# Kernel optimization log

Hardware: AMD Instinct MI355X
Metric: run time of the kernel (lower is better)

## Reference

```python
import jax, jax.numpy as jnp
import numpy as np

H = 16          # num_heads
D = 4           # att_size (hard-coded in module)
HID = 256       # hidden_size
B, N = 4, 1024
SCALE = D ** (-0.5)
BN_EPS = 1e-5
NEG_SLOPE = 0.2


def setup_inputs() -> dict:
    key = jax.random.key(0)
    ks = jax.random.split(key, 12)
    s = 0.05
    return {
        "q": jax.random.normal(ks[0], (B, HID, N), jnp.float32),
        "k": jax.random.normal(ks[1], (B, HID, N), jnp.float32),
        "v": jax.random.normal(ks[2], (B, HID, N), jnp.float32),
        "attn_bias": jax.random.normal(ks[3], (B, H, N, N), jnp.float32),
        # 1x1 Conv1d weights (kernel dim squeezed): [out_ch, in_ch]
        "Wq": jax.random.normal(ks[4], (H * D, HID), jnp.float32) * s,
        "Wk": jax.random.normal(ks[5], (H * D, HID), jnp.float32) * s,
        "Wv": jax.random.normal(ks[6], (H * D, HID), jnp.float32) * s,
        "Wo": jax.random.normal(ks[7], (HID, H * D), jnp.float32) * s,
        "bo": jax.random.normal(ks[8], (HID,), jnp.float32) * s,
        "gamma": jnp.ones((HID,), jnp.float32),
        "beta": jnp.zeros((HID,), jnp.float32),
        "run_mean": jnp.zeros((HID,), jnp.float32),
        "run_var": jnp.ones((HID,), jnp.float32),
    }


def reference(q, k, v, attn_bias, Wq, Wk, Wv, Wo, bo, gamma, beta, run_mean, run_var):
    # 1x1 conv projections: [B, HID, N] -> [B, H*D, N]
    qp = jnp.einsum('oc,bcn->bon', Wq, q)
    kp = jnp.einsum('oc,bcn->bon', Wk, k)
    vp = jnp.einsum('oc,bcn->bon', Wv, v)
    # faithful (non-standard) view: [B, H*D, N] -> [B, D, N, H]
    qh = qp.reshape(B, D, N, H).transpose(0, 3, 2, 1)   # [B, H, N, D]
    vh = vp.reshape(B, D, N, H).transpose(0, 3, 2, 1)   # [B, H, N, D]
    kh = kp.reshape(B, D, N, H).transpose(0, 3, 1, 2)   # [B, H, D, N]
    # scaled dot-product attention with additive bias
    scores = jnp.einsum('bhnd,bhdm->bhnm', qh, kh) * SCALE + attn_bias
    attn = jax.nn.softmax(scores, axis=-1)              # dropout rate 0.0 (eval)
    x = jnp.einsum('bhnm,bhmd->bhnd', attn, vh)         # [B, H, N, D]
    # transpose(3,2) then view(B, H*D, N)
    x = x.transpose(0, 1, 3, 2).reshape(B, H * D, N)
    # output 1x1 conv + BatchNorm1d (eval, running stats) + LeakyReLU(0.2)
    y = jnp.einsum('oc,bcn->bon', Wo, x) + bo[None, :, None]
    inv = jax.lax.rsqrt(run_var + BN_EPS)
    y = (y - run_mean[None, :, None]) * (gamma * inv)[None, :, None] + beta[None, :, None]
    return jnp.where(y > 0, y, NEG_SLOPE * y)
```

## Files before the change

### kernel.cpp

```cpp
#include <hip/hip_runtime.h>

#define HID 256
#define NSEQ 1024
#define NH 16
#define DH 4
#define NB 4
#define SCALEF 0.5f
#define HEADSZ (NB * NH * NSEQ * DH)

typedef float f4 __attribute__((ext_vector_type(4)));

__global__ __launch_bounds__(256) void proj_kernel(
    const float* __restrict__ q, const float* __restrict__ k,
    const float* __restrict__ v, const float* __restrict__ Wq,
    const float* __restrict__ Wk, const float* __restrict__ Wv,
    float* __restrict__ ws)
{
    const int tid   = threadIdx.x;
    const int pos_l = tid & 63;
    int cb = tid >> 6;
    cb = __builtin_amdgcn_readfirstlane(cb);
    const int p    = blockIdx.y;
    const int b    = blockIdx.z;
    const int pos0 = blockIdx.x * 64;

    const float* in = (p == 0) ? q : (p == 1) ? k : v;
    const float* W  = (p == 0) ? Wq : (p == 1) ? Wk : Wv;
    float* dst = ws + (size_t)p * HEADSZ;

    __shared__ float lds_in[64][64];

    float acc[16];
#pragma unroll
    for (int j = 0; j < 16; ++j) acc[j] = 0.f;

    const float* inb = in + (size_t)b * HID * NSEQ;

    for (int chunk = 0; chunk < 4; ++chunk) {
        const int i0 = chunk * 64;
#pragma unroll
        for (int t = 0; t < 16; ++t) {
            int e = tid + t * 256;
            int r = e >> 6, pp = e & 63;
            lds_in[r][pp] = inb[(i0 + r) * NSEQ + pos0 + pp];
        }
        __syncthreads();
#pragma unroll
        for (int i8 = 0; i8 < 64; i8 += 8) {
            float x[8];
#pragma unroll
            for (int j = 0; j < 8; ++j) x[j] = lds_in[i8 + j][pos_l];
#pragma unroll
            for (int kk = 0; kk < 16; ++kk) {
                const float* wr = W + (cb * 16 + kk) * HID + i0 + i8;
#pragma unroll
                for (int j = 0; j < 8; ++j)
                    acc[kk] = fmaf(wr[j], x[j], acc[kk]);
            }
        }
        __syncthreads();
    }

    const int pos_g = pos0 + pos_l;
    const int h     = pos_g & 15;
    const int nsub  = pos_g >> 4;
#pragma unroll
    for (int kk = 0; kk < 16; ++kk) {
        int c = cb * 16 + kk;
        int d = c >> 4;
        int n = (c & 15) * 64 + nsub;
        dst[(((size_t)b * NH + h) * NSEQ + n) * DH + d] = acc[kk];
    }
}

__global__ __launch_bounds__(256, 4) void attn_kernel(
    const float* __restrict__ bias, const float* __restrict__ ws,
    float* __restrict__ x2)
{
    const int tid  = threadIdx.x;
    const int lane = tid & 63;
    const int wave = tid >> 6;
    const int qg   = lane >> 4;
    const int kg   = lane & 15;
    const int h    = blockIdx.y;
    const int b    = blockIdx.z;
    const int n0   = blockIdx.x * 64 + wave * 16;

    const float4* Qh = (const float4*)(ws);
    const float4* Kh = (const float4*)(ws + (size_t)1 * HEADSZ);
    const float4* Vh = (const float4*)(ws + (size_t)2 * HEADSZ);
    const int headbase = (b * NH + h) * NSEQ;

    float4 q4[4];
#pragma unroll
    for (int r = 0; r < 4; ++r) q4[r] = Qh[headbase + n0 + qg * 4 + r];

    float sum[4];
    float o[4][4];
#pragma unroll
    for (int r = 0; r < 4; ++r) {
        sum[r] = 0.f;
#pragma unroll
        for (int d = 0; d < 4; ++d) o[r][d] = 0.f;
    }

    const float* bbase =
        bias + ((size_t)headbase + n0 + qg * 4) * NSEQ + kg * 4;
    const int kvbase = headbase + kg * 4;

#define LOG2E 1.44269504f
#define EOFF  (-16.f * LOG2E)

    for (int m0 = 0; m0 < NSEQ; m0 += 64) {
        f4 bb[4];
#pragma unroll
        for (int r = 0; r < 4; ++r)
            bb[r] = __builtin_nontemporal_load(
                (const f4*)(bbase + (size_t)r * NSEQ + m0));
        float4 kb[4], vb[4];
#pragma unroll
        for (int i = 0; i < 4; ++i) {
            kb[i] = Kh[kvbase + m0 + i];
            vb[i] = Vh[kvbase + m0 + i];
        }
#pragma unroll
        for (int r = 0; r < 4; ++r) {
            const float be[4] = {bb[r].x, bb[r].y, bb[r].z, bb[r].w};
#pragma unroll
            for (int i = 0; i < 4; ++i) {
                float dot = q4[r].x * kb[i].x + q4[r].y * kb[i].y +
                            q4[r].z * kb[i].z + q4[r].w * kb[i].w;
                float s = fmaf(dot, SCALEF, be[i]);
                float e = exp2f(fmaf(s, LOG2E, EOFF));
                sum[r] += e;
                o[r][0] = fmaf(e, vb[i].x, o[r][0]);
                o[r][1] = fmaf(e, vb[i].y, o[r][1]);
                o[r][2] = fmaf(e, vb[i].z, o[r][2]);
                o[r][3] = fmaf(e, vb[i].w, o[r][3]);
            }
        }
    }

#pragma unroll
    for (int st = 1; st <= 8; st <<= 1) {
#pragma unroll
        for (int r = 0; r < 4; ++r) {
            sum[r]  += __shfl_xor(sum[r],  st, 64);
            o[r][0] += __shfl_xor(o[r][0], st, 64);
            o[r][1] += __shfl_xor(o[r][1], st, 64);
            o[r][2] += __shfl_xor(o[r][2], st, 64);
            o[r][3] += __shfl_xor(o[r][3], st, 64);
        }
    }

    if (kg < 4) {
        float4 wv;
        wv.x = o[0][kg] / sum[0];
        wv.y = o[1][kg] / sum[1];
        wv.z = o[2][kg] / sum[2];
        wv.w = o[3][kg] / sum[3];
        *(float4*)(x2 + ((size_t)b * (NH * DH) + h * DH + kg) * NSEQ
                      + n0 + qg * 4) = wv;
    }
}

__global__ __launch_bounds__(256) void out_kernel(
    const float* __restrict__ x2, const float* __restrict__ Wo,
    const float* __restrict__ bo, const float* __restrict__ gamma,
    const float* __restrict__ beta, const float* __restrict__ rmean,
    const float* __restrict__ rvar, float* __restrict__ out)
{
    const int pos = blockIdx.x * 256 + threadIdx.x;
    const int o0  = blockIdx.y * 8;
    const int b   = blockIdx.z;

    float acc[8];
#pragma unroll
    for (int j = 0; j < 8; ++j) acc[j] = 0.f;

    const float* xb = x2 + (size_t)b * (NH * DH) * NSEQ;
#pragma unroll 8
    for (int c = 0; c < NH * DH; ++c) {
        float x = xb[c * NSEQ + pos];
#pragma unroll
        for (int j = 0; j < 8; ++j)
            acc[j] = fmaf(Wo[(o0 + j) * (NH * DH) + c], x, acc[j]);
    }
#pragma unroll
    for (int j = 0; j < 8; ++j) {
        int o = o0 + j;
        float inv = rsqrtf(rvar[o] + 1e-5f);
        float y = acc[j] + bo[o];
        y = (y - rmean[o]) * (gamma[o] * inv) + beta[o];
        y = (y > 0.f) ? y : 0.2f * y;
        out[((size_t)b * HID + o) * NSEQ + pos] = y;
    }
}

extern "C" void kernel_launch(void* const* d_in, const int* in_sizes, int n_in,
                              void* d_out, int out_size, void* d_ws, size_t ws_size,
                              hipStream_t stream) {
    const float* q     = (const float*)d_in[0];
    const float* k     = (const float*)d_in[1];
    const float* v     = (const float*)d_in[2];
    const float* bias  = (const float*)d_in[3];
    const float* Wq    = (const float*)d_in[4];
    const float* Wk    = (const float*)d_in[5];
    const float* Wv    = (const float*)d_in[6];
    const float* Wo    = (const float*)d_in[7];
    const float* bo    = (const float*)d_in[8];
    const float* gamma = (const float*)d_in[9];
    const float* beta  = (const float*)d_in[10];
    const float* rmean = (const float*)d_in[11];
    const float* rvar  = (const float*)d_in[12];

    float* ws = (float*)d_ws;
    float* x2 = ws + (size_t)3 * HEADSZ;
    float* out = (float*)d_out;

    proj_kernel<<<dim3(NSEQ / 64, 3, NB), 256, 0, stream>>>(q, k, v, Wq, Wk, Wv, ws);
    attn_kernel<<<dim3(NSEQ / 64, NH, NB), 256, 0, stream>>>(bias, ws, x2);
    out_kernel<<<dim3(NSEQ / 256, HID / 8, NB), 256, 0, stream>>>(
        x2, Wo, bo, gamma, beta, rmean, rvar, out);
}
```

Baseline: 123.3 us.

## Prefetch bias and projection inputs, vectorize loads in proj and output kernels

The projection kernel now loads its input tile with float4 reads and prefetches the next 64-row chunk into registers while it computes on the current one. The attention kernel double-buffers the attn_bias loads one iteration ahead and lowers the launch-bounds occupancy hint from 4 to 3 to make room for the extra registers. The output kernel is rewritten so each thread handles 4 positions with vector loads and stores across 4 output channels per block. The goal is to hide memory latency on the bandwidth-bound bias stream and to issue fewer, wider memory accesses, at the cost of higher register pressure and lower occupancy in the attention kernel.

New measurement: 135.1 us. 9.6% more time.

```diff
diff --git a/kernel.cpp b/kernel.cpp
--- a/kernel.cpp
+++ b/kernel.cpp
@@ -18,8 +18,7 @@
 {
     const int tid   = threadIdx.x;
     const int pos_l = tid & 63;
-    int cb = tid >> 6;
-    cb = __builtin_amdgcn_readfirstlane(cb);
+    int cb = __builtin_amdgcn_readfirstlane(tid >> 6);
     const int p    = blockIdx.y;
     const int b    = blockIdx.z;
     const int pos0 = blockIdx.x * 64;
@@ -30,21 +29,30 @@
 
     __shared__ float lds_in[64][64];
 
+    const int row_l = tid >> 4;
+    const int col4  = tid & 15;
+    const float* inb = in + (size_t)b * HID * NSEQ + pos0;
+
     float acc[16];
 #pragma unroll
     for (int j = 0; j < 16; ++j) acc[j] = 0.f;
 
-    const float* inb = in + (size_t)b * HID * NSEQ;
-
-    for (int chunk = 0; chunk < 4; ++chunk) {
-        const int i0 = chunk * 64;
-#pragma unroll
-        for (int t = 0; t < 16; ++t) {
-            int e = tid + t * 256;
-            int r = e >> 6, pp = e & 63;
-            lds_in[r][pp] = inb[(i0 + r) * NSEQ + pos0 + pp];
-        }
+    f4 vbuf[4];
+#pragma unroll
+    for (int t = 0; t < 4; ++t)
+        vbuf[t] = *(const f4*)(inb + (size_t)(row_l + 16 * t) * NSEQ + col4 * 4);
+
+    for (int c = 0; c < 4; ++c) {
+#pragma unroll
+        for (int t = 0; t < 4; ++t)
+            *(f4*)&lds_in[row_l + 16 * t][col4 * 4] = vbuf[t];
         __syncthreads();
+        if (c < 3) {
+#pragma unroll
+            for (int t = 0; t < 4; ++t)
+                vbuf[t] = *(const f4*)(inb +
+                    (size_t)((c + 1) * 64 + row_l + 16 * t) * NSEQ + col4 * 4);
+        }
 #pragma unroll
         for (int i8 = 0; i8 < 64; i8 += 8) {
             float x[8];
@@ -52,7 +60,7 @@
             for (int j = 0; j < 8; ++j) x[j] = lds_in[i8 + j][pos_l];
 #pragma unroll
             for (int kk = 0; kk < 16; ++kk) {
-                const float* wr = W + (cb * 16 + kk) * HID + i0 + i8;
+                const float* wr = W + (cb * 16 + kk) * HID + c * 64 + i8;
 #pragma unroll
                 for (int j = 0; j < 8; ++j)
                     acc[kk] = fmaf(wr[j], x[j], acc[kk]);
@@ -73,7 +81,7 @@
     }
 }
 
-__global__ __launch_bounds__(256, 4) void attn_kernel(
+__global__ __launch_bounds__(256, 3) void attn_kernel(
     const float* __restrict__ bias, const float* __restrict__ ws,
     float* __restrict__ x2)
 {
@@ -111,12 +119,18 @@
 #define LOG2E 1.44269504f
 #define EOFF  (-16.f * LOG2E)
 
+    f4 bb[4], bbn[4];
+#pragma unroll
+    for (int r = 0; r < 4; ++r)
+        bb[r] = __builtin_nontemporal_load((const f4*)(bbase + (size_t)r * NSEQ));
+
     for (int m0 = 0; m0 < NSEQ; m0 += 64) {
-        f4 bb[4];
-#pragma unroll
-        for (int r = 0; r < 4; ++r)
-            bb[r] = __builtin_nontemporal_load(
-                (const f4*)(bbase + (size_t)r * NSEQ + m0));
+        if (m0 + 64 < NSEQ) {
+#pragma unroll
+            for (int r = 0; r < 4; ++r)
+                bbn[r] = __builtin_nontemporal_load(
+                    (const f4*)(bbase + (size_t)r * NSEQ + m0 + 64));
+        }
         float4 kb[4], vb[4];
 #pragma unroll
         for (int i = 0; i < 4; ++i) {
@@ -139,6 +153,8 @@
                 o[r][3] = fmaf(e, vb[i].w, o[r][3]);
             }
         }
+#pragma unroll
+        for (int r = 0; r < 4; ++r) bb[r] = bbn[r];
     }
 
 #pragma unroll
@@ -170,30 +186,36 @@
     const float* __restrict__ beta, const float* __restrict__ rmean,
     const float* __restrict__ rvar, float* __restrict__ out)
 {
-    const int pos = blockIdx.x * 256 + threadIdx.x;
-    const int o0  = blockIdx.y * 8;
-    const int b   = blockIdx.z;
-
-    float acc[8];
-#pragma unroll
-    for (int j = 0; j < 8; ++j) acc[j] = 0.f;
+    const int pos4 = threadIdx.x * 4;
+    const int o0   = blockIdx.y * 4;
+    const int b    = blockIdx.z;
 
     const float* xb = x2 + (size_t)b * (NH * DH) * NSEQ;
+
+    f4 acc[4];
+#pragma unroll
+    for (int j = 0; j < 4; ++j) acc[j] = (f4)(0.f);
+
 #pragma unroll 8
     for (int c = 0; c < NH * DH; ++c) {
-        float x = xb[c * NSEQ + pos];
-#pragma unroll
-        for (int j = 0; j < 8; ++j)
-            acc[j] = fmaf(Wo[(o0 + j) * (NH * DH) + c], x, acc[j]);
-    }
-#pragma unroll
-    for (int j = 0; j < 8; ++j) {
-        int o = o0 + j;
-        float inv = rsqrtf(rvar[o] + 1e-5f);
-        float y = acc[j] + bo[o];
-        y = (y - rmean[o]) * (gamma[o] * inv) + beta[o];
-        y = (y > 0.f) ? y : 0.2f * y;
-        out[((size_t)b * HID + o) * NSEQ + pos] = y;
+        f4 x = *(const f4*)(xb + (size_t)c * NSEQ + pos4);
+#pragma unroll
+        for (int j = 0; j < 4; ++j)
+            acc[j] += Wo[(o0 + j) * (NH * DH) + c] * x;
+    }
+#pragma unroll
+    for (int j = 0; j < 4; ++j) {
+        int oc = o0 + j;
+        float scale = gamma[oc] * rsqrtf(rvar[oc] + 1e-5f);
+        f4 y = (acc[j] + (bo[oc] - rmean[oc])) * scale + beta[oc];
+        float* dst = out + ((size_t)b * HID + oc) * NSEQ + pos4;
+        f4 res;
+#pragma unroll
+        for (int d = 0; d < 4; ++d) {
+            float yy = y[d];
+            res[d] = (yy > 0.f) ? yy : 0.2f * yy;
+        }
+        *(f4*)dst = res;
     }
 }
 
@@ -220,6 +242,6 @@
 
     proj_kernel<<<dim3(NSEQ / 64, 3, NB), 256, 0, stream>>>(q, k, v, Wq, Wk, Wv, ws);
     attn_kernel<<<dim3(NSEQ / 64, NH, NB), 256, 0, stream>>>(bias, ws, x2);
-    out_kernel<<<dim3(NSEQ / 256, HID / 8, NB), 256, 0, stream>>>(
+    out_kernel<<<dim3(1, HID / 4, NB), 256, 0, stream>>>(
         x2, Wo, bo, gamma, beta, rmean, rvar, out);
 }
```
